# Kernel optimization log

Hardware: AMD Instinct MI355X
Metric: run time of the kernel (lower is better)

## Reference

```python
import jax, jax.numpy as jnp
import numpy as np

N, T, D = 50000, 16, 4          # nodes, timesteps, input features
E = 800000                      # edges
H, HID = 4, 32                  # GAT heads, hidden dim (concat=False -> mean over heads)
TH, THID = 4, 64                # temporal heads, temporal hidden (= 2*HID)
HD = THID // TH                 # temporal head dim
NEG_SLOPE = 0.2


def setup_inputs() -> dict:
    key = jax.random.key(0)
    ks = iter(jax.random.split(key, 64))
    nrm = lambda shape, s=0.05: jax.random.normal(next(ks), shape, dtype=jnp.float32) * s
    inp = {}
    inp["x"] = jax.random.normal(next(ks), (N, T, D), dtype=jnp.float32)
    inp["edge_index"] = jax.random.randint(next(ks), (2, E), 0, N)
    inp["edge_weight"] = jax.random.uniform(next(ks), (E,), dtype=jnp.float32)
    # input projection
    inp["in_W"], inp["in_b"] = nrm((D, HID)), nrm((HID,))
    # two GATv2 layers (lin_l, lin_r, lin_edge (no bias), att, out bias)
    for i in range(2):
        inp[f"g{i}_Wl"], inp[f"g{i}_bl"] = nrm((HID, H * HID)), nrm((H * HID,))
        inp[f"g{i}_Wr"], inp[f"g{i}_br"] = nrm((HID, H * HID)), nrm((H * HID,))
        inp[f"g{i}_We"] = nrm((1, H * HID))
        inp[f"g{i}_att"] = nrm((H, HID))
        inp[f"g{i}_bias"] = nrm((HID,))
    # temporal attention block
    inp["Wq"], inp["bq"] = nrm((HID, THID)), nrm((THID,))
    inp["Wk"], inp["bk"] = nrm((HID, THID)), nrm((THID,))
    inp["Wv"], inp["bv"] = nrm((HID, THID)), nrm((THID,))
    inp["Wo"], inp["bo"] = nrm((THID, HID)), nrm((HID,))
    # heads
    inp["fW1"], inp["fb1"] = nrm((HID, 32)), nrm((32,))
    inp["fW2"], inp["fb2"] = nrm((32, 1)), nrm((1,))
    inp["rW1"], inp["rb1"] = nrm((HID, 32)), nrm((32,))
    inp["rW2"], inp["rb2"] = nrm((32, 1)), nrm((1,))
    return inp


def _gatv2(xp, edge_index, edge_attr, Wl, bl, Wr, br, We, att, bias):
    """GATv2Conv, heads=H, concat=False (mean), edge_dim=1, no self loops."""
    src, dst = edge_index[0], edge_index[1]          # message src -> dst
    xl = (xp @ Wl + bl).reshape(N, H, HID)
    xr = (xp @ Wr + br).reshape(N, H, HID)
    ee = (edge_attr @ We).reshape(E, H, HID)
    m = xl[src] + xr[dst] + ee                       # (E,H,C)
    m = jnp.where(m > 0, m, NEG_SLOPE * m)           # leaky_relu
    logits = jnp.einsum('ehc,hc->eh', m, att)        # (E,H)
    mx = jax.ops.segment_max(logits, dst, num_segments=N)
    mx = jnp.where(jnp.isfinite(mx), mx, 0.0)
    a = jnp.exp(logits - mx[dst])
    denom = jax.ops.segment_sum(a, dst, num_segments=N)
    alpha = a / (denom[dst] + 1e-16)                 # segment softmax over dst
    out = jax.ops.segment_sum(alpha[:, :, None] * xl[src], dst, num_segments=N)
    return out.mean(axis=1) + bias                   # (N,HID)


def reference(x, edge_index, edge_weight,
              in_W, in_b,
              g0_Wl, g0_bl, g0_Wr, g0_br, g0_We, g0_att, g0_bias,
              g1_Wl, g1_bl, g1_Wr, g1_br, g1_We, g1_att, g1_bias,
              Wq, bq, Wk, bk, Wv, bv, Wo, bo,
              fW1, fb1, fW2, fb2, rW1, rb1, rW2, rb2):
    edge_attr = edge_weight[:, None]                 # (E,1)
    x_seq = x @ in_W + in_b                          # (N,T,HID)
    x_pool = x_seq.mean(axis=1)                      # (N,HID)
    x_pool = jax.nn.relu(_gatv2(x_pool, edge_index, edge_attr,
                                g0_Wl, g0_bl, g0_Wr, g0_br, g0_We, g0_att, g0_bias))
    x_pool = jax.nn.relu(_gatv2(x_pool, edge_index, edge_attr,
                                g1_Wl, g1_bl, g1_Wr, g1_br, g1_We, g1_att, g1_bias))
    x_seq = x_seq + x_pool[:, None, :]
    node_reps = jnp.transpose(x_seq, (1, 0, 2))      # (T,N,HID)

    def heads(z):                                    # (T,N,THID) -> (N,TH,T,HD)
        return jnp.transpose(z.reshape(T, N, TH, HD), (1, 2, 0, 3))
    Qh = heads(node_reps @ Wq + bq)
    Kh = heads(node_reps @ Wk + bk)
    Vh = heads(node_reps @ Wv + bv)
    scale = HD ** -0.5
    scores = jnp.einsum('bhtd,bhsd->bhts', Qh, Kh) * scale
    w = jax.nn.softmax(scores, axis=-1)
    ctx = jnp.einsum('bhts,bhsd->bhtd', w, Vh)       # (N,TH,T,HD)
    ctx = jnp.transpose(ctx, (2, 0, 1, 3)).reshape(T, N, THID)
    temporal_out = ctx @ Wo + bo                     # (T,N,HID)

    last = temporal_out[-1]                          # (N,HID)
    forecast = jax.nn.relu(jax.nn.relu(last @ fW1 + fb1) @ fW2 + fb2)   # (N,1)
    risk = jax.nn.sigmoid(jax.nn.relu(last @ rW1 + rb1) @ rW2 + rb2)    # (N,1)
    return forecast, risk, temporal_out
```

## Files before the change

### kernel.cpp

```cpp
#include <hip/hip_runtime.h>
#include <hip/hip_bf16.h>

#define NN 50000
#define TT 16
#define DD 4
#define EE 800000
#define HH 4
#define HID 32
#define THID 64
#define HD 16

typedef __attribute__((ext_vector_type(8))) short bf16x8;
typedef __attribute__((ext_vector_type(4))) float f32x4;
typedef __attribute__((ext_vector_type(2))) float f32x2;
typedef __attribute__((ext_vector_type(4))) unsigned u32x4;
typedef __attribute__((ext_vector_type(4))) _Float16 h4;

__device__ __forceinline__ unsigned short f2bf(float f){
    unsigned u = __float_as_uint(f);
    u = u + 0x7fffu + ((u >> 16) & 1u);
    return (unsigned short)(u >> 16);
}
__device__ __forceinline__ unsigned cvtpk(float a, float b){
    unsigned r;
    asm("v_cvt_pk_bf16_f32 %0, %1, %2" : "=v"(r) : "v"(a), "v"(b));
    return r;
}
__device__ __forceinline__ bf16x8 mk8(unsigned a0, unsigned a1, unsigned a2, unsigned a3){
    u32x4 u = {a0, a1, a2, a3};
    return __builtin_bit_cast(bf16x8, u);
}
__device__ __forceinline__ bf16x8 gather8(int d0, int d1, int s0, int s1, bool zero){
    int a0 = __shfl(d0, s0, 64);
    int a1 = __shfl(d1, s0, 64);
    int a2 = __shfl(d0, s1, 64);
    int a3 = __shfl(d1, s1, 64);
    if (zero){ a0 = 0; a1 = 0; a2 = 0; a3 = 0; }
    return mk8((unsigned)a0, (unsigned)a1, (unsigned)a2, (unsigned)a3);
}

__global__ __launch_bounds__(256) void pool_kernel(const float* __restrict__ x,
        const float* __restrict__ in_W, const float* __restrict__ in_b,
        float* __restrict__ xp){
    __shared__ float xs[512];
    __shared__ float xb[8][4];
    int tid = threadIdx.x;
    size_t base = (size_t)blockIdx.x * 512;
    xs[tid]       = x[base + tid];
    xs[tid + 256] = x[base + tid + 256];
    __syncthreads();
    if (tid < 32){
        int nl = tid >> 2, d = tid & 3;
        float s = 0.f;
        #pragma unroll
        for (int t = 0; t < 16; t++) s += xs[nl*64 + t*4 + d];
        xb[nl][d] = s * (1.f/16.f);
    }
    __syncthreads();
    int nl = tid >> 5, c = tid & 31;
    float v = in_b[c];
    #pragma unroll
    for (int d = 0; d < 4; d++) v += xb[nl][d] * in_W[d*32 + c];
    xp[(size_t)(blockIdx.x*8 + nl)*32 + c] = v;
}

__global__ void wfrag_kernel(const float* __restrict__ Wq, const float* __restrict__ Wk,
                             const float* __restrict__ Wv, const float* __restrict__ Wo,
                             unsigned short* __restrict__ frag){
    int fid = blockIdx.x, lane = threadIdx.x;
    const float* W; int b, k0, ncol;
    if (fid < 4)      { W = Wq; b = fid;      k0 = 0;  ncol = 64; }
    else if (fid < 8) { W = Wk; b = fid - 4;  k0 = 0;  ncol = 64; }
    else if (fid < 12){ W = Wv; b = fid - 8;  k0 = 0;  ncol = 64; }
    else { W = Wo; int rb = (fid-12) >> 1, ks = (fid-12) & 1; b = rb; k0 = ks*32; ncol = 32; }
    int col = 16*b + (lane & 15);
    int kk  = k0 + (lane >> 4)*8;
    unsigned short* out = frag + ((size_t)fid*64 + lane)*8;
    #pragma unroll
    for (int j = 0; j < 8; j++) out[j] = f2bf(W[(size_t)(kk + j)*ncol + col]);
}

__global__ void count_kernel(const int* __restrict__ ei, int* __restrict__ counts){
    int e = blockIdx.x*256 + threadIdx.x;
    if (e >= EE) return;
    atomicAdd(&counts[ei[EE + e]], 1);
}

#define SBLK 49

__global__ __launch_bounds__(256) void bsum_kernel(const int* __restrict__ counts,
                                                   int* __restrict__ bsum){
    int b = blockIdx.x, tid = threadIdx.x;
    int base = b*1024 + tid*4;
    int s = 0;
    if (base + 3 < NN){ int4 v = *(const int4*)(counts + base); s = v.x+v.y+v.z+v.w; }
    else { for (int i = 0; i < 4; i++) if (base+i < NN) s += counts[base+i]; }
    #pragma unroll
    for (int off = 1; off < 64; off <<= 1) s += __shfl_xor(s, off, 64);
    __shared__ int wsum[4];
    if ((tid & 63) == 0) wsum[tid >> 6] = s;
    __syncthreads();
    if (tid == 0) bsum[b] = wsum[0] + wsum[1] + wsum[2] + wsum[3];
}

__global__ __launch_bounds__(256) void scan2_kernel(const int* __restrict__ counts,
                                                    const int* __restrict__ bsum,
                                                    int* __restrict__ offs,
                                                    int* __restrict__ nxt){
    int b = blockIdx.x, tid = threadIdx.x;
    __shared__ int lds[256];
    __shared__ int bofs_s;
    if (tid < 64){
        int v = (tid < b) ? bsum[tid] : 0;
        #pragma unroll
        for (int off = 1; off < 64; off <<= 1) v += __shfl_xor(v, off, 64);
        if (tid == 0) bofs_s = v;
    }
    int base = b*1024 + tid*4;
    int c0=0, c1=0, c2=0, c3=0;
    if (base + 3 < NN){ int4 v = *(const int4*)(counts + base); c0=v.x; c1=v.y; c2=v.z; c3=v.w; }
    else {
        if (base   < NN) c0 = counts[base];
        if (base+1 < NN) c1 = counts[base+1];
        if (base+2 < NN) c2 = counts[base+2];
        if (base+3 < NN) c3 = counts[base+3];
    }
    lds[tid] = c0 + c1 + c2 + c3;
    __syncthreads();
    for (int off = 1; off < 256; off <<= 1){
        int v = (tid >= off) ? lds[tid - off] : 0;
        __syncthreads();
        lds[tid] += v;
        __syncthreads();
    }
    int run = bofs_s + ((tid == 0) ? 0 : lds[tid - 1]);
    if (base   < NN){ offs[base]   = run; nxt[base]   = run; } run += c0;
    if (base+1 < NN){ offs[base+1] = run; nxt[base+1] = run; } run += c1;
    if (base+2 < NN){ offs[base+2] = run; nxt[base+2] = run; } run += c2;
    if (base+3 < NN){ offs[base+3] = run; nxt[base+3] = run; }
    if (b == 0 && tid == 0) offs[NN] = EE;
}

__global__ void fill_kernel(const int* __restrict__ ei, const float* __restrict__ ew,
                            int* __restrict__ nxt, int2* __restrict__ esrc){
    int e = blockIdx.x*256 + threadIdx.x;
    if (e >= EE) return;
    int dst = ei[EE + e];
    int pos = atomicAdd(&nxt[dst], 1);
    esrc[pos] = make_int2(ei[e], __float_as_int(ew[e]));
}

#define LNODES 8
__global__ __launch_bounds__(128) void linlr_kernel(const float* __restrict__ xp,
        const float* __restrict__ Wl, const float* __restrict__ bl,
        const float* __restrict__ Wr, const float* __restrict__ br,
        _Float16* __restrict__ xlh, _Float16* __restrict__ xrh){
    int j = threadIdx.x;
    int n0 = blockIdx.x * LNODES;
    float wl[32], wrr[32];
    #pragma unroll
    for (int k = 0; k < 32; k++){ wl[k] = Wl[k*128 + j]; wrr[k] = Wr[k*128 + j]; }
    float blv = bl[j], brv = br[j];
    __shared__ float xs[LNODES][32];
    int r = j >> 5, c = j & 31;
    #pragma unroll
    for (int q = 0; q < LNODES/4; q++)
        xs[q*4 + r][c] = xp[(size_t)(n0 + q*4 + r)*32 + c];
    __syncthreads();
    #pragma unroll
    for (int m = 0; m < LNODES; m++){
        float al = blv, ar = brv;
        #pragma unroll
        for (int k = 0; k < 32; k++){ float v = xs[m][k]; al += v*wl[k]; ar += v*wrr[k]; }
        xlh[(size_t)(n0+m)*128 + j] = (_Float16)al;
        xrh[(size_t)(n0+m)*128 + j] = (_Float16)ar;
    }
}

__global__ __launch_bounds__(256) void gat_fused_kernel(
        const int* __restrict__ offs, const int2* __restrict__ esrc,
        const _Float16* __restrict__ xlh, const _Float16* __restrict__ xrh,
        const float* __restrict__ We, const float* __restrict__ att,
        const float* __restrict__ bias, float* __restrict__ xq){
    int n = blockIdx.x;
    int tid = threadIdx.x;
    int w = tid >> 6, lane = tid & 63;
    int half = lane >> 5, l2 = lane & 31;
    int cb = (l2 >> 3)*32 + (l2 & 7)*4;

    h4 xr4 = __builtin_bit_cast(h4, *(const f32x2*)(xrh + (size_t)n*128 + cb));
    f32x4 wef = {We[cb], We[cb+1], We[cb+2], We[cb+3]};
    h4 We4 = {(_Float16)wef[0], (_Float16)wef[1], (_Float16)wef[2], (_Float16)wef[3]};
    f32x4 atf = {att[cb], att[cb+1], att[cb+2], att[cb+3]};
    h4 at4 = {(_Float16)atf[0], (_Float16)atf[1], (_Float16)atf[2], (_Float16)atf[3]};

    int beg = offs[n], end = offs[n+1];
    float acc0 = 0.f, acc1 = 0.f, acc2 = 0.f, acc3 = 0.f, den = 0.f;
    for (int i = beg + 2*w; i < end; i += 8){
        int e = i + half;
        bool valid = e < end;
        int ec = valid ? e : end - 1;
        int2 r = esrc[ec];
        int src  = r.x;
        float wt = __int_as_float(r.y);
        h4 xl4 = __builtin_bit_cast(h4, *(const f32x2*)(xlh + (size_t)src*128 + cb));
        h4 m = xl4 + xr4 + We4 * (_Float16)wt;
        h4 rr = __builtin_elementwise_max(m, m * (_Float16)0.2f);
        h4 zp = at4 * rr;
        float z = (float)zp[0] + (float)zp[1] + (float)zp[2] + (float)zp[3];
        z += __shfl_xor(z, 1);
        z += __shfl_xor(z, 2);
        z += __shfl_xor(z, 4);
        float a = valid ? __expf(z) : 0.f;
        den  += a;
        acc0 += a * (float)xl4[0];
        acc1 += a * (float)xl4[1];
        acc2 += a * (float)xl4[2];
        acc3 += a * (float)xl4[3];
    }
    __shared__ float lacc[4][64][4];
    __shared__ float lden[4][64];
    lacc[w][lane][0] = acc0;
    lacc[w][lane][1] = acc1;
    lacc[w][lane][2] = acc2;
    lacc[w][lane][3] = acc3;
    lden[w][lane] = den;
    __syncthreads();
    if (tid < 32){
        int j = tid;
        float s = 0.f;
        #pragma unroll
        for (int h = 0; h < 4; h++){
            int lb = h*8 + (j >> 2);
            int sub = j & 3;
            float av = 0.f, dv = 0.f;
            #pragma unroll
            for (int ww = 0; ww < 4; ww++){
                av += lacc[ww][lb][sub] + lacc[ww][lb + 32][sub];
                dv += lden[ww][lb] + lden[ww][lb + 32];
            }
            s += av / (dv + 1e-16f);
        }
        s = s*0.25f + bias[j];
        xq[(size_t)n*32 + j] = fmaxf(s, 0.f);
    }
}

__global__ __launch_bounds__(256) void temporal_kernel(const float* __restrict__ x,
        const float* __restrict__ xpool,
        const float* __restrict__ in_W, const float* __restrict__ in_b,
        const float* __restrict__ bq, const float* __restrict__ bk,
        const float* __restrict__ bv, const float* __restrict__ bo,
        const unsigned short* __restrict__ wfrag,
        float* __restrict__ out2){
    __shared__ float ctxL[4][64][18];
    int tid = threadIdx.x, w = tid >> 6, lane = tid & 63;
    int n = blockIdx.x*4 + w;
    int t = lane & 15, g = lane >> 4;
    int k0 = g * 8;

    f32x4 xv  = *(const f32x4*)(x + (size_t)n*64 + t*4);
    f32x4 ib0 = *(const f32x4*)(in_b + k0);
    f32x4 ib1 = *(const f32x4*)(in_b + k0 + 4);
    f32x4 xp0 = *(const f32x4*)(xpool + (size_t)n*32 + k0);
    f32x4 xp1 = *(const f32x4*)(xpool + (size_t)n*32 + k0 + 4);
    f32x4 iw0a = *(const f32x4*)(in_W + k0),      iw0b = *(const f32x4*)(in_W + k0 + 4);
    f32x4 iw1a = *(const f32x4*)(in_W + 32 + k0), iw1b = *(const f32x4*)(in_W + 32 + k0 + 4);
    f32x4 iw2a = *(const f32x4*)(in_W + 64 + k0), iw2b = *(const f32x4*)(in_W + 64 + k0 + 4);
    f32x4 iw3a = *(const f32x4*)(in_W + 96 + k0), iw3b = *(const f32x4*)(in_W + 96 + k0 + 4);
    f32x4 sA = ib0 + xp0 + xv[0]*iw0a + xv[1]*iw1a + xv[2]*iw2a + xv[3]*iw3a;
    f32x4 sB = ib1 + xp1 + xv[0]*iw0b + xv[1]*iw1b + xv[2]*iw2b + xv[3]*iw3b;
    bf16x8 sfrag = mk8(cvtpk(sA[0],sA[1]), cvtpk(sA[2],sA[3]), cvtpk(sB[0],sB[1]), cvtpk(sB[2],sB[3]));

    const bf16x8* WF = (const bf16x8*)wfrag;
    f32x4 zero = {0.f, 0.f, 0.f, 0.f};

    int qd0[4], qd1[4], kd0[4], kd1[4], vd0[4], vd1[4];
    #pragma unroll
    for (int b = 0; b < 4; b++){
        bf16x8 wq = WF[(0*4 + b)*64 + lane];
        bf16x8 wk = WF[(1*4 + b)*64 + lane];
        bf16x8 wv = WF[(2*4 + b)*64 + lane];
        f32x4 qc = __builtin_amdgcn_mfma_f32_16x16x32_bf16(wq, sfrag, zero, 0, 0, 0);
        f32x4 kc = __builtin_amdgcn_mfma_f32_16x16x32_bf16(wk, sfrag, zero, 0, 0, 0);
        f32x4 vc = __builtin_amdgcn_mfma_f32_16x16x32_bf16(sfrag, wv, zero, 0, 0, 0);
        f32x4 bq4 = *(const f32x4*)(bq + 16*b + 4*g);
        f32x4 bk4 = *(const f32x4*)(bk + 16*b + 4*g);
        float bvv = bv[16*b + t];
        qc += bq4; kc += bk4;
        vc[0] += bvv; vc[1] += bvv; vc[2] += bvv; vc[3] += bvv;
        qd0[b] = (int)cvtpk(qc[0], qc[1]); qd1[b] = (int)cvtpk(qc[2], qc[3]);
        kd0[b] = (int)cvtpk(kc[0], kc[1]); kd1[b] = (int)cvtpk(kc[2], kc[3]);
        vd0[b] = (int)cvtpk(vc[0], vc[1]); vd1[b] = (int)cvtpk(vc[2], vc[3]);
    }

    int s0l = t + 32*(g & 1);
    int s1l = s0l + 16;
    bool hiz = (g >= 2);
    #pragma unroll
    for (int h = 0; h < 4; h++){
        bf16x8 ka = gather8(kd0[h], kd1[h], s0l, s1l, hiz);
        bf16x8 qb = gather8(qd0[h], qd1[h], s0l, s1l, false);
        f32x4 sc = __builtin_amdgcn_mfma_f32_16x16x32_bf16(ka, qb, zero, 0, 0, 0);
        sc *= 0.25f;
        float m = fmaxf(fmaxf(sc[0], sc[1]), fmaxf(sc[2], sc[3]));
        m = fmaxf(m, __shfl_xor(m, 16, 64));
        m = fmaxf(m, __shfl_xor(m, 32, 64));
        float p0 = __expf(sc[0] - m), p1 = __expf(sc[1] - m);
        float p2 = __expf(sc[2] - m), p3 = __expf(sc[3] - m);
        float sum = p0 + p1 + p2 + p3;
        sum += __shfl_xor(sum, 16, 64);
        sum += __shfl_xor(sum, 32, 64);
        float inv = 1.f / sum;
        int pd0 = (int)cvtpk(p0, p1), pd1 = (int)cvtpk(p2, p3);
        bf16x8 va = gather8(vd0[h], vd1[h], s0l, s1l, hiz);
        bf16x8 pb = gather8(pd0, pd1, s0l, s1l, false);
        f32x4 cx = __builtin_amdgcn_mfma_f32_16x16x32_bf16(va, pb, zero, 0, 0, 0);
        cx *= inv;
        #pragma unroll
        for (int r = 0; r < 4; r++) ctxL[w][h*16 + 4*g + r][t] = cx[r];
    }

    bf16x8 cb[2];
    #pragma unroll
    for (int ks = 0; ks < 2; ks++){
        float c0 = ctxL[w][ks*32 + k0 + 0][t], c1 = ctxL[w][ks*32 + k0 + 1][t];
        float c2 = ctxL[w][ks*32 + k0 + 2][t], c3 = ctxL[w][ks*32 + k0 + 3][t];
        float c4 = ctxL[w][ks*32 + k0 + 4][t], c5 = ctxL[w][ks*32 + k0 + 5][t];
        float c6 = ctxL[w][ks*32 + k0 + 6][t], c7 = ctxL[w][ks*32 + k0 + 7][t];
        cb[ks] = mk8(cvtpk(c0,c1), cvtpk(c2,c3), cvtpk(c4,c5), cvtpk(c6,c7));
    }
    #pragma unroll
    for (int rb = 0; rb < 2; rb++){
        bf16x8 wo0 = WF[(12 + rb*2 + 0)*64 + lane];
        bf16x8 wo1 = WF[(12 + rb*2 + 1)*64 + lane];
        f32x4 oc = __builtin_amdgcn_mfma_f32_16x16x32_bf16(wo0, cb[0], zero, 0, 0, 0);
        oc = __builtin_amdgcn_mfma_f32_16x16x32_bf16(wo1, cb[1], oc, 0, 0, 0);
        f32x4 bo4 = *(const f32x4*)(bo + 16*rb + 4*g);
        oc += bo4;
        #pragma unroll
        for (int r = 0; r < 4; r++) ctxL[w][16*rb + 4*g + r][t] = oc[r];
    }
    float o[8];
    #pragma unroll
    for (int j = 0; j < 8; j++) o[j] = ctxL[w][g*8 + j][t];
    float* outp = out2 + ((size_t)t*NN + n)*32 + g*8;
    *(f32x4*)outp       = (f32x4){o[0], o[1], o[2], o[3]};
    *((f32x4*)outp + 1) = (f32x4){o[4], o[5], o[6], o[7]};
}

__global__ __launch_bounds__(256) void head_kernel(const float* __restrict__ out2,
        const float* __restrict__ fW1, const float* __restrict__ fb1,
        const float* __restrict__ fW2, const float* __restrict__ fb2,
        const float* __restrict__ rW1, const float* __restrict__ rb1,
        const float* __restrict__ rW2, const float* __restrict__ rb2,
        float* __restrict__ out0, float* __restrict__ out1){
    int tid = threadIdx.x;
    int wv = tid >> 6, lane = tid & 63;
    int n = blockIdx.x*4 + wv;
    int c = lane & 31, path = lane >> 5;
    const float* W1 = path ? rW1 : fW1;
    const float* b1 = path ? rb1 : fb1;
    const float* W2 = path ? rW2 : fW2;
    const float* b2 = path ? rb2 : fb2;
    const float* last = out2 + ((size_t)15*NN + n)*32;
    float h1 = b1[c];
    #pragma unroll
    for (int k = 0; k < 32; k++) h1 += last[k] * W1[k*32 + c];
    h1 = fmaxf(h1, 0.f);
    float z = h1 * W2[c];
    #pragma unroll
    for (int off = 16; off >= 1; off >>= 1) z += __shfl_xor(z, off, 64);
    if (lane == 0)  out0[n] = fmaxf(z + b2[0], 0.f);
    if (lane == 32) out1[n] = 1.f / (1.f + __expf(-(z + b2[0])));
}

extern "C" void kernel_launch(void* const* d_in, const int* in_sizes, int n_in,
                              void* d_out, int out_size, void* d_ws, size_t ws_size,
                              hipStream_t stream){
    const float* x    = (const float*)d_in[0];
    const int*   ei   = (const int*)  d_in[1];
    const float* ew   = (const float*)d_in[2];
    const float* in_W = (const float*)d_in[3];
    const float* in_b = (const float*)d_in[4];
    const float* Wq = (const float*)d_in[19];
    const float* bq = (const float*)d_in[20];
    const float* Wk = (const float*)d_in[21];
    const float* bk = (const float*)d_in[22];
    const float* Wv = (const float*)d_in[23];
    const float* bv = (const float*)d_in[24];
    const float* Wo = (const float*)d_in[25];
    const float* bo = (const float*)d_in[26];
    const float* fW1 = (const float*)d_in[27];
    const float* fb1 = (const float*)d_in[28];
    const float* fW2 = (const float*)d_in[29];
    const float* fb2 = (const float*)d_in[30];
    const float* rW1 = (const float*)d_in[31];
    const float* rb1 = (const float*)d_in[32];
    const float* rW2 = (const float*)d_in[33];
    const float* rb2 = (const float*)d_in[34];

    float* out0 = (float*)d_out;
    float* out1 = out0 + NN;
    float* out2 = out0 + 2*NN;

    float* ws = (float*)d_ws;
    size_t off = 0;
    _Float16* xlh = (_Float16*)(ws + off); off += (size_t)NN*64;
    _Float16* xrh = (_Float16*)(ws + off); off += (size_t)NN*64;
    float* xpA    = ws + off; off += (size_t)NN*32;
    float* xpB    = ws + off; off += (size_t)NN*32;
    int* counts   = (int*)(ws + off); off += NN;
    int* offs     = (int*)(ws + off); off += NN + 1;
    int* nxt      = (int*)(ws + off); off += NN + 1;
    int* bsum     = (int*)(ws + off); off += SBLK;
    off = (off + 1) & ~(size_t)1;
    int2* esrc    = (int2*)(ws + off); off += (size_t)EE*2;
    off = (off + 3) & ~(size_t)3;
    unsigned short* wfrag = (unsigned short*)(ws + off); off += 16*64*8/2;

    hipMemsetAsync(counts, 0, NN*sizeof(int), stream);
    pool_kernel<<<NN/8, 256, 0, stream>>>(x, in_W, in_b, xpA);
    wfrag_kernel<<<16, 64, 0, stream>>>(Wq, Wk, Wv, Wo, wfrag);
    count_kernel<<<(EE+255)/256, 256, 0, stream>>>(ei, counts);
    bsum_kernel<<<SBLK, 256, 0, stream>>>(counts, bsum);
    scan2_kernel<<<SBLK, 256, 0, stream>>>(counts, bsum, offs, nxt);
    fill_kernel<<<(EE+255)/256, 256, 0, stream>>>(ei, ew, nxt, esrc);

    for (int layer = 0; layer < 2; layer++){
        const float* Wl   = (const float*)d_in[5 + 7*layer];
        const float* bl   = (const float*)d_in[6 + 7*layer];
        const float* Wr   = (const float*)d_in[7 + 7*layer];
        const float* br   = (const float*)d_in[8 + 7*layer];
        const float* We   = (const float*)d_in[9 + 7*layer];
        const float* att  = (const float*)d_in[10 + 7*layer];
        const float* bias = (const float*)d_in[11 + 7*layer];
        const float* xin  = layer ? xpB : xpA;
        float*       xout = layer ? xpA : xpB;
        linlr_kernel<<<NN/LNODES, 128, 0, stream>>>(xin, Wl, bl, Wr, br, xlh, xrh);
        gat_fused_kernel<<<NN, 256, 0, stream>>>(offs, esrc, xlh, xrh, We, att, bias, xout);
    }

    temporal_kernel<<<NN/4, 256, 0, stream>>>(x, xpA, in_W, in_b,
                                              bq, bk, bv, bo, wfrag, out2);
    head_kernel<<<NN/4, 256, 0, stream>>>(out2, fW1, fb1, fW2, fb2,
                                          rW1, rb1, rW2, rb2, out0, out1);
}
```

Measured before the change: 396.6 us.

## Store GAT source projections in FP8 and fuse output heads into temporal kernel

The lin_l projection used for the random per-edge gather is now stored as FP8 (e4m3) instead of FP16, which halves the bytes fetched per edge in the GAT aggregation kernel. Each gathered value is decoded with the packed FP8-to-f32 conversion instructions. Separately, the forecast and risk MLP heads are fused into the temporal kernel and read the last timestep from shared memory, which removes one launch and a re-read of the output. FP8 storage sharply reduces precision of the attention inputs and the aggregated features, so accuracy tolerance is a risk.

```diff
diff --git a/kernel.cpp b/kernel.cpp
--- a/kernel.cpp
+++ b/kernel.cpp
@@ -154,7 +154,7 @@
 __global__ __launch_bounds__(128) void linlr_kernel(const float* __restrict__ xp,
         const float* __restrict__ Wl, const float* __restrict__ bl,
         const float* __restrict__ Wr, const float* __restrict__ br,
-        _Float16* __restrict__ xlh, _Float16* __restrict__ xrh){
+        unsigned char* __restrict__ xlf, _Float16* __restrict__ xrh){
     int j = threadIdx.x;
     int n0 = blockIdx.x * LNODES;
     float wl[32], wrr[32];
@@ -172,14 +172,15 @@
         float al = blv, ar = brv;
         #pragma unroll
         for (int k = 0; k < 32; k++){ float v = xs[m][k]; al += v*wl[k]; ar += v*wrr[k]; }
-        xlh[(size_t)(n0+m)*128 + j] = (_Float16)al;
+        unsigned p8 = __builtin_amdgcn_cvt_pk_fp8_f32(al, al, 0u, false);
+        xlf[(size_t)(n0+m)*128 + j] = (unsigned char)(p8 & 0xffu);
         xrh[(size_t)(n0+m)*128 + j] = (_Float16)ar;
     }
 }
 
 __global__ __launch_bounds__(256) void gat_fused_kernel(
         const int* __restrict__ offs, const int2* __restrict__ esrc,
-        const _Float16* __restrict__ xlh, const _Float16* __restrict__ xrh,
+        const unsigned char* __restrict__ xlf, const _Float16* __restrict__ xrh,
         const float* __restrict__ We, const float* __restrict__ att,
         const float* __restrict__ bias, float* __restrict__ xq){
     int n = blockIdx.x;
@@ -203,7 +204,10 @@
         int2 r = esrc[ec];
         int src  = r.x;
         float wt = __int_as_float(r.y);
-        h4 xl4 = __builtin_bit_cast(h4, *(const f32x2*)(xlh + (size_t)src*128 + cb));
+        unsigned u = *(const unsigned*)(xlf + (size_t)src*128 + cb);
+        f32x2 lo = __builtin_amdgcn_cvt_pk_f32_fp8(u, false);
+        f32x2 hi = __builtin_amdgcn_cvt_pk_f32_fp8(u, true);
+        h4 xl4 = {(_Float16)lo[0], (_Float16)lo[1], (_Float16)hi[0], (_Float16)hi[1]};
         h4 m = xl4 + xr4 + We4 * (_Float16)wt;
         h4 rr = __builtin_elementwise_max(m, m * (_Float16)0.2f);
         h4 zp = at4 * rr;
@@ -213,10 +217,10 @@
         z += __shfl_xor(z, 4);
         float a = valid ? __expf(z) : 0.f;
         den  += a;
-        acc0 += a * (float)xl4[0];
-        acc1 += a * (float)xl4[1];
-        acc2 += a * (float)xl4[2];
-        acc3 += a * (float)xl4[3];
+        acc0 += a * lo[0];
+        acc1 += a * lo[1];
+        acc2 += a * hi[0];
+        acc3 += a * hi[1];
     }
     __shared__ float lacc[4][64][4];
     __shared__ float lden[4][64];
@@ -252,6 +256,11 @@
         const float* __restrict__ bq, const float* __restrict__ bk,
         const float* __restrict__ bv, const float* __restrict__ bo,
         const unsigned short* __restrict__ wfrag,
+        const float* __restrict__ fW1, const float* __restrict__ fb1,
+        const float* __restrict__ fW2, const float* __restrict__ fb2,
+        const float* __restrict__ rW1, const float* __restrict__ rb1,
+        const float* __restrict__ rW2, const float* __restrict__ rb2,
+        float* __restrict__ out0, float* __restrict__ out1,
         float* __restrict__ out2){
     __shared__ float ctxL[4][64][18];
     int tid = threadIdx.x, w = tid >> 6, lane = tid & 63;
@@ -347,32 +356,21 @@
     float* outp = out2 + ((size_t)t*NN + n)*32 + g*8;
     *(f32x4*)outp       = (f32x4){o[0], o[1], o[2], o[3]};
     *((f32x4*)outp + 1) = (f32x4){o[4], o[5], o[6], o[7]};
-}
-
-__global__ __launch_bounds__(256) void head_kernel(const float* __restrict__ out2,
-        const float* __restrict__ fW1, const float* __restrict__ fb1,
-        const float* __restrict__ fW2, const float* __restrict__ fb2,
-        const float* __restrict__ rW1, const float* __restrict__ rb1,
-        const float* __restrict__ rW2, const float* __restrict__ rb2,
-        float* __restrict__ out0, float* __restrict__ out1){
-    int tid = threadIdx.x;
-    int wv = tid >> 6, lane = tid & 63;
-    int n = blockIdx.x*4 + wv;
-    int c = lane & 31, path = lane >> 5;
-    const float* W1 = path ? rW1 : fW1;
-    const float* b1 = path ? rb1 : fb1;
-    const float* W2 = path ? rW2 : fW2;
-    const float* b2 = path ? rb2 : fb2;
-    const float* last = out2 + ((size_t)15*NN + n)*32;
-    float h1 = b1[c];
-    #pragma unroll
-    for (int k = 0; k < 32; k++) h1 += last[k] * W1[k*32 + c];
+
+    int cc = lane & 31, path = lane >> 5;
+    const float* W1  = path ? rW1 : fW1;
+    const float* b1v = path ? rb1 : fb1;
+    const float* W2  = path ? rW2 : fW2;
+    const float* b2v = path ? rb2 : fb2;
+    float h1 = b1v[cc];
+    #pragma unroll
+    for (int k = 0; k < 32; k++) h1 += ctxL[w][k][15] * W1[k*32 + cc];
     h1 = fmaxf(h1, 0.f);
-    float z = h1 * W2[c];
-    #pragma unroll
-    for (int off = 16; off >= 1; off >>= 1) z += __shfl_xor(z, off, 64);
-    if (lane == 0)  out0[n] = fmaxf(z + b2[0], 0.f);
-    if (lane == 32) out1[n] = 1.f / (1.f + __expf(-(z + b2[0])));
+    float z = h1 * W2[cc];
+    #pragma unroll
+    for (int off2 = 16; off2 >= 1; off2 >>= 1) z += __shfl_xor(z, off2, 64);
+    if (lane == 0)  out0[n] = fmaxf(z + b2v[0], 0.f);
+    if (lane == 32) out1[n] = 1.f / (1.f + __expf(-(z + b2v[0])));
 }
 
 extern "C" void kernel_launch(void* const* d_in, const int* in_sizes, int n_in,
@@ -406,7 +404,7 @@
 
     float* ws = (float*)d_ws;
     size_t off = 0;
-    _Float16* xlh = (_Float16*)(ws + off); off += (size_t)NN*64;
+    unsigned char* xlf = (unsigned char*)(ws + off); off += (size_t)NN*32;
     _Float16* xrh = (_Float16*)(ws + off); off += (size_t)NN*64;
     float* xpA    = ws + off; off += (size_t)NN*32;
     float* xpB    = ws + off; off += (size_t)NN*32;
@@ -437,12 +435,12 @@
         const float* bias = (const float*)d_in[11 + 7*layer];
         const float* xin  = layer ? xpB : xpA;
         float*       xout = layer ? xpA : xpB;
-        linlr_kernel<<<NN/LNODES, 128, 0, stream>>>(xin, Wl, bl, Wr, br, xlh, xrh);
-        gat_fused_kernel<<<NN, 256, 0, stream>>>(offs, esrc, xlh, xrh, We, att, bias, xout);
+        linlr_kernel<<<NN/LNODES, 128, 0, stream>>>(xin, Wl, bl, Wr, br, xlf, xrh);
+        gat_fused_kernel<<<NN, 256, 0, stream>>>(offs, esrc, xlf, xrh, We, att, bias, xout);
     }
 
     temporal_kernel<<<NN/4, 256, 0, stream>>>(x, xpA, in_W, in_b,
-                                              bq, bk, bv, bo, wfrag, out2);
-    head_kernel<<<NN/4, 256, 0, stream>>>(out2, fW1, fb1, fW2, fb2,
-                                          rW1, rb1, rW2, rb2, out0, out1);
-}
+                                              bq, bk, bv, bo, wfrag,
+                                              fW1, fb1, fW2, fb2, rW1, rb1, rW2, rb2,
+                                              out0, out1, out2);
+}
```

Result: faster. 382.1 us (-3.6%).
